# Kernel tuning notes

Hardware: AMD Instinct MI355X
Metric: run time of the kernel (lower is better)

The kernel has to match this reference:

```python
import jax, jax.numpy as jnp
import numpy as np
from jax import lax

B, C, H, W = 4, 32, 512, 512
DN = ('NCHW', 'OIHW', 'NCHW')

# cv2 correlation kernels (filter2D/Sobel/Scharr do correlation, not convolution)
SOBEL_X = np.array([[-1, 0, 1], [-2, 0, 2], [-1, 0, 1]], np.float32)
SOBEL_Y = SOBEL_X.T
SCHARR_X = np.array([[-3, 0, 3], [-10, 0, 10], [-3, 0, 3]], np.float32)
SCHARR_Y = SCHARR_X.T
LAPLACE3 = np.array([[2, 0, 2], [0, -8, 0], [2, 0, 2]], np.float32)  # cv2.Laplacian ksize=3
ROBERTS_X = np.array([[-1, 0], [0, 1]], np.float32)
ROBERTS_Y = np.array([[0, -1], [1, 0]], np.float32)
PREWITT_X = np.array([[1, 1, 1], [0, 0, 0], [-1, -1, -1]], np.float32)
PREWITT_Y = np.array([[-1, 0, 1], [-1, 0, 1], [-1, 0, 1]], np.float32)


def _corr(x, k, pad_hw):
    # per-channel 2D correlation with cv2 BORDER_REFLECT_101 padding
    b, c, h, w = x.shape
    xp = jnp.pad(x, ((0, 0), (0, 0), pad_hw[0], pad_hw[1]), mode='reflect')
    kj = jnp.asarray(k)[None, None]  # (1,1,kh,kw)
    y = lax.conv_general_dilated(xp.reshape(b * c, 1, xp.shape[2], xp.shape[3]),
                                 kj, (1, 1), 'VALID', dimension_numbers=DN)
    return y.reshape(b, c, h, w)


def _norm(x):
    # Norm(): per-sample zero-mean/unit-std over all of (C,H,W)
    m = jnp.mean(x, axis=(1, 2, 3), keepdims=True)
    s = jnp.std(x, axis=(1, 2, 3), keepdims=True)
    return (x - m) / s


def get_operator(x):
    p3 = ((1, 1), (1, 1))          # 3x3 kernel, anchor (1,1)
    p2 = ((1, 0), (1, 0))          # 2x2 kernel, cv2 default anchor (1,1)
    b1 = _norm(0.5 * _corr(x, SOBEL_X, p3) + 0.5 * _corr(x, SOBEL_Y, p3))
    b2 = _norm(0.5 * _corr(x, SCHARR_X, p3) + 0.5 * _corr(x, SCHARR_Y, p3))
    b3 = _norm(_corr(x, LAPLACE3, p3))
    b4 = _norm(0.5 * _corr(x, ROBERTS_X, p2) + 0.5 * _corr(x, ROBERTS_Y, p2))
    b5 = _norm(0.5 * _corr(x, PREWITT_X, p3) + 0.5 * _corr(x, PREWITT_Y, p3))
    return jnp.concatenate([b1, b2, b3, b4, b5], axis=1)


def conv3x3(x, w, b):
    y = lax.conv_general_dilated(x, w, (1, 1), [(1, 1), (1, 1)], dimension_numbers=DN)
    return y + b[None, :, None, None]


def maxpool2(x):
    b, c, h, w = x.shape
    return x.reshape(b, c, h // 2, 2, w // 2, 2).max(axis=(3, 5))


def deconv2x2(x, w, b):
    # ConvTranspose2d(k=2, s=2): each pixel expands to a 2x2 block; w is (Cin,Cout,2,2)
    bb, ci, h, wd = x.shape
    y = jnp.einsum('bihw,iopq->bohpwq', x, w).reshape(bb, w.shape[1], 2 * h, 2 * wd)
    return y + b[None, :, None, None]


def setup_inputs():
    key = jax.random.key(0)
    ks = jax.random.split(key, 24)
    def uni(k, shape, fan_in):
        bd = 1.0 / np.sqrt(fan_in)
        return jax.random.uniform(k, shape, jnp.float32, -bd, bd)
    d = {'x': jax.random.normal(ks[0], (B, C, H, W), jnp.float32)}
    d['conv1_w'] = uni(ks[1], (C, 5 * C, 3, 3), 5 * C * 9)
    d['conv1_b'] = uni(ks[2], (C,), 5 * C * 9)
    for i, name in enumerate(['conv2', 'conv3', 'conv4', 'conv5', 'conv6', 'conv7']):
        d[name + '_w'] = uni(ks[3 + 2 * i], (C, C, 3, 3), C * 9)
        d[name + '_b'] = uni(ks[4 + 2 * i], (C,), C * 9)
    for i, name in enumerate(['deconv1', 'deconv2', 'deconv3']):
        d[name + '_w'] = uni(ks[15 + 2 * i], (C, C, 2, 2), C * 4)
        d[name + '_b'] = uni(ks[16 + 2 * i], (C,), C * 4)
    return d


def reference(x, conv1_w, conv1_b, conv2_w, conv2_b, conv3_w, conv3_b, conv4_w, conv4_b,
              conv5_w, conv5_b, conv6_w, conv6_b, conv7_w, conv7_b,
              deconv1_w, deconv1_b, deconv2_w, deconv2_b, deconv3_w, deconv3_b):
    orig = x
    y = get_operator(x)                      # (B, 5C, H, W)
    y = conv3x3(y, conv1_w, conv1_b)
    y = maxpool2(y)
    y = conv3x3(y, conv2_w, conv2_b)
    y = maxpool2(y)
    y = conv3x3(y, conv3_w, conv3_b)
    y = maxpool2(y)
    y = conv3x3(y, conv4_w, conv4_b)
    y = deconv2x2(y, deconv1_w, deconv1_b)   # sizes divide evenly -> no interpolate
    y = conv3x3(y, conv5_w, conv5_b)
    y = deconv2x2(y, deconv2_w, deconv2_b)
    y = conv3x3(y, conv6_w, conv6_b)
    y = deconv2x2(y, deconv3_w, deconv3_b)
    y = conv3x3(y, conv7_w, conv7_b)
    return orig * y
```

## Files before the change

kernel.cpp:

```cpp
#include <hip/hip_runtime.h>
#include <hip/hip_bf16.h>
#include <cstddef>


typedef unsigned short u16;
typedef unsigned int uint;
typedef __attribute__((ext_vector_type(8))) short short8v;
typedef __attribute__((ext_vector_type(4))) float float4v;

constexpr int Bn = 4, Cn = 32, Hn = 512, Wn = 512;
constexpr int PLANE = Hn * Wn;

__device__ __forceinline__ u16 f2b(float f) {
  union { float f; uint i; } c; c.f = f;
  uint r = c.i + 0x7FFFu + ((c.i >> 16) & 1u);
  return (u16)(r >> 16);
}

static __device__ __forceinline__ int reflect_idx(int i, int n) {
  return i < 0 ? -i : (i >= n ? 2 * n - 2 - i : i);
}

#define BRANCH_VALS(n00, n01, n02, n10, n11, n12, n20, n21, n22, v1, v2, v3, v4, v5)        \
  do {                                                                                      \
    v1 = -(n00 + n01 + n10) + (n12 + n21 + n22);                                            \
    v2 = -3.f * n00 - 5.f * n01 - 5.f * n10 + 5.f * n12 + 5.f * n21 + 3.f * n22;            \
    v3 = 2.f * (n00 + n02 + n20 + n22) - 8.f * n11;                                         \
    v4 = 0.5f * (-n00 - n01 + n10 + n11);                                                   \
    v5 = 0.5f * n01 + n02 - 0.5f * n10 + 0.5f * n12 - n20 - 0.5f * n21;                     \
  } while (0)

__global__ void __launch_bounds__(128) k_opstats(const float* __restrict__ x,
                                                 float* __restrict__ partS,
                                                 float* __restrict__ partQ) {
  int bid = blockIdx.x;
  int b = bid >> 11;
  int local = bid & 2047;
  int c = local >> 6;
  int chunk = local & 63;
  int t = threadIdx.x;
  int w0 = t * 4;
  const float* xp = x + (size_t)(b * Cn + c) * PLANE;
  int h0 = chunk * 8;

  int ci[6];
#pragma unroll
  for (int j = 0; j < 6; j++) ci[j] = reflect_idx(w0 - 1 + j, Wn);

  float ap[6], ac[6], an[6];
  {
    const float* rp = xp + reflect_idx(h0 - 1, Hn) * Wn;
#pragma unroll
    for (int j = 0; j < 6; j++) ap[j] = rp[ci[j]];
  }
  {
    const float* rp = xp + h0 * Wn;
#pragma unroll
    for (int j = 0; j < 6; j++) ac[j] = rp[ci[j]];
  }

  float s[5] = {0, 0, 0, 0, 0}, q[5] = {0, 0, 0, 0, 0};
#pragma unroll
  for (int r = 0; r < 8; ++r) {
    int h = h0 + r;
    const float* rp = xp + reflect_idx(h + 1, Hn) * Wn;
#pragma unroll
    for (int j = 0; j < 6; j++) an[j] = rp[ci[j]];
#pragma unroll
    for (int k = 0; k < 4; ++k) {
      float v1, v2, v3, v4, v5;
      BRANCH_VALS(ap[k], ap[k + 1], ap[k + 2], ac[k], ac[k + 1], ac[k + 2],
                  an[k], an[k + 1], an[k + 2], v1, v2, v3, v4, v5);
      s[0] += v1; q[0] += v1 * v1;
      s[1] += v2; q[1] += v2 * v2;
      s[2] += v3; q[2] += v3 * v3;
      s[3] += v4; q[3] += v4 * v4;
      s[4] += v5; q[5 - 1] += v5 * v5;
    }
#pragma unroll
    for (int j = 0; j < 6; j++) { ap[j] = ac[j]; ac[j] = an[j]; }
  }

#pragma unroll
  for (int i = 0; i < 5; i++) {
    float ss = s[i], qq = q[i];
#pragma unroll
    for (int off = 32; off > 0; off >>= 1) {
      ss += __shfl_down(ss, off);
      qq += __shfl_down(qq, off);
    }
    if ((t & 63) == 0) {
      int wv = t >> 6;
      int g = b * 5 + i;
      int idx = (c * 64 + chunk) * 2 + wv;
      partS[(size_t)g * 4096 + idx] = ss;
      partQ[(size_t)g * 4096 + idx] = qq;
    }
  }
}

__global__ void __launch_bounds__(256) k_stats(const float* __restrict__ partS,
                                               const float* __restrict__ partQ,
                                               float* __restrict__ stats) {
  __shared__ float red[256];
  int g = blockIdx.x;
  int t = threadIdx.x;
  float ss = 0.f, qq = 0.f;
  const float* ps = partS + (size_t)g * 4096;
  const float* pq = partQ + (size_t)g * 4096;
  for (int i = t; i < 4096; i += 256) {
    ss += ps[i];
    qq += pq[i];
  }
  red[t] = ss;
  __syncthreads();
  for (int o = 128; o > 0; o >>= 1) {
    if (t < o) red[t] += red[t + o];
    __syncthreads();
  }
  float S = red[0];
  __syncthreads();
  red[t] = qq;
  __syncthreads();
  for (int o = 128; o > 0; o >>= 1) {
    if (t < o) red[t] += red[t + o];
    __syncthreads();
  }
  if (t == 0) {
    const float N = 8388608.0f;
    float mean = S / N;
    float var = red[0] / N - mean * mean;
    stats[g * 2] = mean;
    stats[g * 2 + 1] = 1.0f / sqrtf(var);
  }
}

__global__ void __launch_bounds__(256) k_opfused(const float* __restrict__ x, int b,
                                                 u16* __restrict__ opm) {
  __shared__ u16 lin[160 * 66];
  int t = threadIdx.x;
  int px = t & 63, cg = t >> 6;
  int h = blockIdx.y;
  int w = blockIdx.x * 64 + px;
  int hm = h == 0 ? 1 : h - 1, hp = h == 511 ? 510 : h + 1;
  int wm = w == 0 ? 1 : w - 1, wp = w == 511 ? 510 : w + 1;

#pragma unroll
  for (int it = 0; it < 8; ++it) {
    int c = it * 4 + cg;
    const float* xp = x + ((size_t)(b * 32 + c) * 512) * 512;
    const float* r0 = xp + (size_t)hm * 512;
    const float* r1 = xp + (size_t)h * 512;
    const float* r2 = xp + (size_t)hp * 512;
    float n00 = r0[wm], n01 = r0[w], n02 = r0[wp];
    float n10 = r1[wm], n11 = r1[w], n12 = r1[wp];
    float n20 = r2[wm], n21 = r2[w], n22 = r2[wp];
    float v1, v2, v3, v4, v5;
    BRANCH_VALS(n00, n01, n02, n10, n11, n12, n20, n21, n22, v1, v2, v3, v4, v5);
    lin[(c) * 66 + px] = f2b(v1);
    lin[(32 + c) * 66 + px] = f2b(v2);
    lin[(64 + c) * 66 + px] = f2b(v3);
    lin[(96 + c) * 66 + px] = f2b(v4);
    lin[(128 + c) * 66 + px] = f2b(v5);
  }
  __syncthreads();

  size_t obase = ((size_t)h * 512 + blockIdx.x * 64) * 160;
#pragma unroll
  for (int i = 0; i < 5; ++i) {
    int u = t + i * 256;
    int pxi = u / 20, chg = u % 20;
    u16 tmp[8];
#pragma unroll
    for (int j = 0; j < 8; ++j) tmp[j] = lin[(chg * 8 + j) * 66 + pxi];
    *(uint4*)&opm[obase + (size_t)pxi * 160 + chg * 8] = *(uint4*)tmp;
  }
}

__global__ void __launch_bounds__(256) k_prep_shared(
    const float* w2, const float* w3, const float* w4, const float* w5,
    const float* w6, const float* w7, const float* dw1, const float* dw2,
    const float* dw3, u16* A2, u16* A3, u16* A4, u16* A5, u16* A6, u16* A7,
    u16* Ad1, u16* Ad2, u16* Ad3) {
  int id = blockIdx.x * 256 + threadIdx.x;
  if (id < 55296) {
    int s = id / 9216, r = id % 9216;
    int tap = r / 1024, oc = (r >> 5) & 31, ic = r & 31;
    const float* w = s == 0 ? w2 : s == 1 ? w3 : s == 2 ? w4 : s == 3 ? w5 : s == 4 ? w6 : w7;
    u16* A = s == 0 ? A2 : s == 1 ? A3 : s == 2 ? A4 : s == 3 ? A5 : s == 4 ? A6 : A7;
    A[r] = f2b(w[(oc * 32 + ic) * 9 + tap]);
  } else if (id < 67584) {
    int r = id - 55296;
    int s = r / 4096, e = r % 4096;
    int par = e >> 10, oc = (e >> 5) & 31, ic = e & 31;
    const float* w = s == 0 ? dw1 : s == 1 ? dw2 : dw3;
    u16* A = s == 0 ? Ad1 : s == 1 ? Ad2 : Ad3;
    A[e] = f2b(w[(ic * 32 + oc) * 4 + par]);
  }
}

__global__ void __launch_bounds__(256) k_prep_b_all(const float* __restrict__ w1,
                                                    const float* __restrict__ b1,
                                                    const float* __restrict__ stats,
                                                    u16* __restrict__ A1all,
                                                    float* __restrict__ bias1all) {
  int e = blockIdx.x * 256 + threadIdx.x;
  if (e < 184320) {
    int b = e / 46080, r = e % 46080;
    int br = r / 9216, r2 = r % 9216;
    int tap = r2 / 1024, oc = (r2 >> 5) & 31, ic = r2 & 31;
    A1all[e] = f2b(w1[(oc * 160 + br * 32 + ic) * 9 + tap] * stats[(b * 5 + br) * 2 + 1]);
  } else if (e < 184448) {
    int t2 = e - 184320;
    int b = t2 >> 5, oc = t2 & 31;
    float s = 0.f;
    for (int ch = 0; ch < 160; ++ch) {
      int br = ch >> 5;
      float mi = stats[(b * 5 + br) * 2] * stats[(b * 5 + br) * 2 + 1];
      const float* wp = w1 + (size_t)(oc * 160 + ch) * 9;
      float ws = 0.f;
#pragma unroll
      for (int tap = 0; tap < 9; ++tap) ws += wp[tap];
      s += ws * mi;
    }
    bias1all[b * 32 + oc] = b1[oc] - s;
  }
}

template <int CIN, int MODE>
__global__ void __launch_bounds__(256) k_conv_mfma(const u16* __restrict__ in,
                                                   const u16* __restrict__ Aw,
                                                   const float* __restrict__ bias,
                                                   u16* __restrict__ outb,
                                                   float* __restrict__ outf,
                                                   const float* __restrict__ xorig,
                                                   int H, int W) {
  constexpr int ICC = CIN / 32;
  __shared__ __align__(16) char smem[(MODE == 1) ? 32768 : 20736];
  u16* bs = (u16*)smem;
  int t = threadIdx.x;
  int l = t & 63, wv = t >> 6;
  int ln = l & 15, q = l >> 4;
  int bz = blockIdx.z;
  int h0 = blockIdx.y * 16, w0 = blockIdx.x * 16;

  float4v acc[4][2];
#pragma unroll
  for (int i = 0; i < 4; ++i) {
    acc[i][0] = (float4v){0.f, 0.f, 0.f, 0.f};
    acc[i][1] = (float4v){0.f, 0.f, 0.f, 0.f};
  }

  for (int icc = 0; icc < ICC; ++icc) {
    for (int u = t; u < 1296; u += 256) {
      int px = u >> 2, sq = u & 3;
      int ry = px / 18, rx = px - ry * 18;
      int gh = h0 - 1 + ry, gw = w0 - 1 + rx;
      uint4 v = {0, 0, 0, 0};
      if (gh >= 0 && gh < H && gw >= 0 && gw < W)
        v = *(const uint4*)&in[(((size_t)bz * H + gh) * W + gw) * CIN + icc * 32 + sq * 8];
      *(uint4*)((char*)bs + px * 64 + ((sq ^ (px & 3)) << 4)) = v;
    }
    short8v af[9][2];
#pragma unroll
    for (int tp = 0; tp < 9; ++tp) {
      af[tp][0] = *(const short8v*)&Aw[((size_t)(icc * 9 + tp) * 32 + ln) * 32 + q * 8];
      af[tp][1] = *(const short8v*)&Aw[((size_t)(icc * 9 + tp) * 32 + 16 + ln) * 32 + q * 8];
    }
    __syncthreads();
#pragma unroll
    for (int r4 = 0; r4 < 4; ++r4) {
      int r = wv * 4 + r4;
#pragma unroll
      for (int dy = 0; dy < 3; ++dy) {
#pragma unroll
        for (int dx = 0; dx < 3; ++dx) {
          int px = (r + dy) * 18 + ln + dx;
          short8v bf = *(const short8v*)((const char*)bs + px * 64 + ((q ^ (px & 3)) << 4));
          acc[r4][0] = __builtin_amdgcn_mfma_f32_16x16x32_bf16(af[dy * 3 + dx][0], bf, acc[r4][0], 0, 0, 0);
          acc[r4][1] = __builtin_amdgcn_mfma_f32_16x16x32_bf16(af[dy * 3 + dx][1], bf, acc[r4][1], 0, 0, 0);
        }
      }
    }
    if (ICC > 1) __syncthreads();
  }

  if (MODE == 0) {
#pragma unroll
    for (int r4 = 0; r4 < 4; ++r4) {
      int h = h0 + wv * 4 + r4;
      int wpix = w0 + ln;
#pragma unroll
      for (int g = 0; g < 2; ++g) {
        float v0 = acc[r4][g][0] + bias[g * 16 + q * 4 + 0];
        float v1 = acc[r4][g][1] + bias[g * 16 + q * 4 + 1];
        float v2 = acc[r4][g][2] + bias[g * 16 + q * 4 + 2];
        float v3 = acc[r4][g][3] + bias[g * 16 + q * 4 + 3];
        uint2 pk;
        pk.x = (uint)f2b(v0) | ((uint)f2b(v1) << 16);
        pk.y = (uint)f2b(v2) | ((uint)f2b(v3) << 16);
        *(uint2*)&outb[(((size_t)bz * H + h) * W + wpix) * 32 + g * 16 + q * 4] = pk;
      }
    }
  } else if (MODE == 2) {
    int Hp = H >> 1, Wp = W >> 1;
#pragma unroll
    for (int rp = 0; rp < 2; ++rp) {
#pragma unroll
      for (int g = 0; g < 2; ++g) {
        float m0 = fmaxf(acc[2 * rp][g][0], acc[2 * rp + 1][g][0]);
        float m1 = fmaxf(acc[2 * rp][g][1], acc[2 * rp + 1][g][1]);
        float m2 = fmaxf(acc[2 * rp][g][2], acc[2 * rp + 1][g][2]);
        float m3 = fmaxf(acc[2 * rp][g][3], acc[2 * rp + 1][g][3]);
        m0 = fmaxf(m0, __shfl_xor(m0, 1));
        m1 = fmaxf(m1, __shfl_xor(m1, 1));
        m2 = fmaxf(m2, __shfl_xor(m2, 1));
        m3 = fmaxf(m3, __shfl_xor(m3, 1));
        if (!(l & 1)) {
          int ph = (h0 >> 1) + wv * 2 + rp;
          int pw = (w0 >> 1) + (ln >> 1);
          uint2 pk;
          pk.x = (uint)f2b(m0 + bias[g * 16 + q * 4 + 0]) |
                 ((uint)f2b(m1 + bias[g * 16 + q * 4 + 1]) << 16);
          pk.y = (uint)f2b(m2 + bias[g * 16 + q * 4 + 2]) |
                 ((uint)f2b(m3 + bias[g * 16 + q * 4 + 3]) << 16);
          *(uint2*)&outb[(((size_t)bz * Hp + ph) * Wp + pw) * 32 + g * 16 + q * 4] = pk;
        }
      }
    }
  } else {
    float* os = (float*)smem;
    __syncthreads();
#pragma unroll
    for (int r4 = 0; r4 < 4; ++r4) {
      int hl = wv * 4 + r4;
#pragma unroll
      for (int g = 0; g < 2; ++g) {
#pragma unroll
        for (int i = 0; i < 4; ++i) {
          int oc = g * 16 + q * 4 + i;
          os[(oc * 16 + hl) * 16 + ln] = acc[r4][g][i] + bias[oc];
        }
      }
    }
    __syncthreads();
#pragma unroll
    for (int j = 0; j < 8; ++j) {
      int u = t + j * 256;
      int wq = u & 3, hh = (u >> 2) & 15, oc = u >> 6;
      float4v v = *(const float4v*)&os[(oc * 16 + hh) * 16 + wq * 4];
      size_t gidx = (((size_t)bz * 32 + oc) * H + h0 + hh) * W + w0 + wq * 4;
      float4v xo = *(const float4v*)&xorig[gidx];
      v[0] *= xo[0]; v[1] *= xo[1]; v[2] *= xo[2]; v[3] *= xo[3];
      *(float4v*)&outf[gidx] = v;
    }
  }
}

__global__ void __launch_bounds__(256) k_deconv_mfma(const u16* __restrict__ in,
                                                     const u16* __restrict__ Aw,
                                                     const float* __restrict__ bias,
                                                     u16* __restrict__ out,
                                                     int Hi, int Wi) {
  int t = threadIdx.x;
  int l = t & 63, wv = t >> 6, ln = l & 15, q = l >> 4;
  int z = blockIdx.z, b = z >> 2, par = z & 3, p = par >> 1, qpar = par & 1;
  int h0 = blockIdx.y * 16, w0 = blockIdx.x * 16;
  int Ho = Hi * 2, Wo = Wi * 2;
  short8v af0 = *(const short8v*)&Aw[((size_t)par * 32 + ln) * 32 + q * 8];
  short8v af1 = *(const short8v*)&Aw[((size_t)par * 32 + 16 + ln) * 32 + q * 8];
#pragma unroll
  for (int r4 = 0; r4 < 4; ++r4) {
    int h = h0 + wv * 4 + r4;
    short8v bf = *(const short8v*)&in[(((size_t)b * Hi + h) * Wi + w0 + ln) * 32 + q * 8];
    float4v a0 = (float4v){0.f, 0.f, 0.f, 0.f};
    float4v a1 = (float4v){0.f, 0.f, 0.f, 0.f};
    a0 = __builtin_amdgcn_mfma_f32_16x16x32_bf16(af0, bf, a0, 0, 0, 0);
    a1 = __builtin_amdgcn_mfma_f32_16x16x32_bf16(af1, bf, a1, 0, 0, 0);
    int oh = 2 * h + p, ow = 2 * (w0 + ln) + qpar;
    size_t ob = (((size_t)b * Ho + oh) * Wo + ow) * 32;
    uint2 pk;
    pk.x = (uint)f2b(a0[0] + bias[q * 4 + 0]) | ((uint)f2b(a0[1] + bias[q * 4 + 1]) << 16);
    pk.y = (uint)f2b(a0[2] + bias[q * 4 + 2]) | ((uint)f2b(a0[3] + bias[q * 4 + 3]) << 16);
    *(uint2*)&out[ob + q * 4] = pk;
    pk.x = (uint)f2b(a1[0] + bias[16 + q * 4 + 0]) | ((uint)f2b(a1[1] + bias[16 + q * 4 + 1]) << 16);
    pk.y = (uint)f2b(a1[2] + bias[16 + q * 4 + 2]) | ((uint)f2b(a1[3] + bias[16 + q * 4 + 3]) << 16);
    *(uint2*)&out[ob + 16 + q * 4] = pk;
  }
}

extern "C" void kernel_launch(void* const* d_in, const int* in_sizes, int n_in,
                              void* d_out, int out_size, void* d_ws, size_t ws_size,
                              hipStream_t stream) {
  const float* x   = (const float*)d_in[0];
  const float* w1  = (const float*)d_in[1];
  const float* b1  = (const float*)d_in[2];
  const float* w2  = (const float*)d_in[3];
  const float* b2  = (const float*)d_in[4];
  const float* w3  = (const float*)d_in[5];
  const float* b3  = (const float*)d_in[6];
  const float* w4  = (const float*)d_in[7];
  const float* b4  = (const float*)d_in[8];
  const float* w5  = (const float*)d_in[9];
  const float* b5  = (const float*)d_in[10];
  const float* w6  = (const float*)d_in[11];
  const float* b6  = (const float*)d_in[12];
  const float* w7  = (const float*)d_in[13];
  const float* b7  = (const float*)d_in[14];
  const float* dw1 = (const float*)d_in[15];
  const float* db1 = (const float*)d_in[16];
  const float* dw2 = (const float*)d_in[17];
  const float* db2 = (const float*)d_in[18];
  const float* dw3 = (const float*)d_in[19];
  const float* db3 = (const float*)d_in[20];
  float* out = (float*)d_out;
  char* wsb = (char*)d_ws;

  u16* opm   = (u16*)(wsb + 0);
  u16* p1    = (u16*)(wsb + 83886080ull);
  u16* p2    = (u16*)(wsb + 100663296ull);
  u16* p3    = (u16*)(wsb + 104857600ull);
  u16* t4    = (u16*)(wsb + 105906176ull);
  u16* dc1   = (u16*)(wsb + 106954752ull);
  u16* t5    = (u16*)(wsb + 111149056ull);
  u16* dc2   = (u16*)(wsb + 115343360ull);
  u16* t6    = (u16*)(wsb + 132120576ull);
  u16* dc3   = (u16*)(wsb + 148897792ull);
  u16* A1all = (u16*)(wsb + 216006656ull);
  u16* A2    = (u16*)(wsb + 216375296ull);
  u16* A3    = (u16*)(wsb + 216393728ull);
  u16* A4    = (u16*)(wsb + 216412160ull);
  u16* A5    = (u16*)(wsb + 216430592ull);
  u16* A6    = (u16*)(wsb + 216449024ull);
  u16* A7    = (u16*)(wsb + 216467456ull);
  u16* Ad1   = (u16*)(wsb + 216485888ull);
  u16* Ad2   = (u16*)(wsb + 216494080ull);
  u16* Ad3   = (u16*)(wsb + 216502272ull);
  float* bias1all = (float*)(wsb + 216510464ull);
  float* partS    = (float*)(wsb + 216510976ull);
  float* partQ    = (float*)(wsb + 216838656ull);
  float* stats    = (float*)(wsb + 217166336ull);

  k_prep_shared<<<264, 256, 0, stream>>>(w2, w3, w4, w5, w6, w7, dw1, dw2, dw3,
                                         A2, A3, A4, A5, A6, A7, Ad1, Ad2, Ad3);
  k_opstats<<<8192, 128, 0, stream>>>(x, partS, partQ);
  k_stats<<<20, 256, 0, stream>>>(partS, partQ, stats);
  k_prep_b_all<<<721, 256, 0, stream>>>(w1, b1, stats, A1all, bias1all);

  for (int b = 0; b < 4; ++b) {
    k_opfused<<<dim3(8, 512), 256, 0, stream>>>(x, b, opm);
    k_conv_mfma<160, 2><<<dim3(32, 32, 1), 256, 0, stream>>>(
        opm, A1all + (size_t)b * 46080, bias1all + b * 32,
        p1 + (size_t)b * 256 * 256 * 32, nullptr, nullptr, 512, 512);
  }

  k_conv_mfma<32, 2><<<dim3(16, 16, 4), 256, 0, stream>>>(p1, A2, b2, p2, nullptr, nullptr, 256, 256);
  k_conv_mfma<32, 2><<<dim3(8, 8, 4), 256, 0, stream>>>(p2, A3, b3, p3, nullptr, nullptr, 128, 128);
  k_conv_mfma<32, 0><<<dim3(4, 4, 4), 256, 0, stream>>>(p3, A4, b4, t4, nullptr, nullptr, 64, 64);
  k_deconv_mfma<<<dim3(4, 4, 16), 256, 0, stream>>>(t4, Ad1, db1, dc1, 64, 64);
  k_conv_mfma<32, 0><<<dim3(8, 8, 4), 256, 0, stream>>>(dc1, A5, b5, t5, nullptr, nullptr, 128, 128);
  k_deconv_mfma<<<dim3(8, 8, 16), 256, 0, stream>>>(t5, Ad2, db2, dc2, 128, 128);
  k_conv_mfma<32, 0><<<dim3(16, 16, 4), 256, 0, stream>>>(dc2, A6, b6, t6, nullptr, nullptr, 256, 256);
  k_deconv_mfma<<<dim3(16, 16, 16), 256, 0, stream>>>(t6, Ad3, db3, dc3, 256, 256);
  k_conv_mfma<32, 1><<<dim3(32, 32, 4), 256, 0, stream>>>(dc3, A7, b7, nullptr, out, x, 512, 512);
}
```

Baseline: 791.0 us.

## Fold edge-operator branches into conv1 as a single 5x5 conv on input

The five fixed edge filters are composed algebraically with conv1's 3x3 weights into one 5x5 kernel (32→32 channels) per batch, so conv1 reads x directly instead of materialising the 160-channel bf16 operator map. Normalization is folded into the weights and bias. Border pixels, where the composition does not hold, are recomputed exactly by a separate scalar kernel that overwrites them. The final conv's epilogue now stages output in two halves to reduce shared memory. This removes a large intermediate write and read, but relies on the separate border correction and changes rounding, since weights are composed before the bf16 cast.

```diff
diff --git a/kernel.cpp b/kernel.cpp
--- a/kernel.cpp
+++ b/kernel.cpp
@@ -11,6 +11,9 @@
 constexpr int Bn = 4, Cn = 32, Hn = 512, Wn = 512;
 constexpr int PLANE = Hn * Wn;
 
+__device__ __forceinline__ float b2f(u16 u) {
+  union { uint i; float f; } c; c.i = ((uint)u) << 16; return c.f;
+}
 __device__ __forceinline__ u16 f2b(float f) {
   union { float f; uint i; } c; c.f = f;
   uint r = c.i + 0x7FFFu + ((c.i >> 16) & 1u);
@@ -29,6 +32,13 @@
     v4 = 0.5f * (-n00 - n01 + n10 + n11);                                                   \
     v5 = 0.5f * n01 + n02 - 0.5f * n10 + 0.5f * n12 - n20 - 0.5f * n21;                     \
   } while (0)
+
+__device__ const float Sdev[5][9] = {
+    {-1.f, -1.f, 0.f, -1.f, 0.f, 1.f, 0.f, 1.f, 1.f},
+    {-3.f, -5.f, 0.f, -5.f, 0.f, 5.f, 0.f, 5.f, 3.f},
+    {2.f, 0.f, 2.f, 0.f, -8.f, 0.f, 2.f, 0.f, 2.f},
+    {-0.5f, -0.5f, 0.f, 0.5f, 0.5f, 0.f, 0.f, 0.f, 0.f},
+    {0.f, 0.5f, 1.f, -0.5f, 0.f, 0.5f, -1.f, -0.5f, 0.f}};
 
 __global__ void __launch_bounds__(128) k_opstats(const float* __restrict__ x,
                                                  float* __restrict__ partS,
@@ -75,7 +85,7 @@
       s[1] += v2; q[1] += v2 * v2;
       s[2] += v3; q[2] += v3 * v3;
       s[3] += v4; q[3] += v4 * v4;
-      s[4] += v5; q[5 - 1] += v5 * v5;
+      s[4] += v5; q[4] += v5 * v5;
     }
 #pragma unroll
     for (int j = 0; j < 6; j++) { ap[j] = ac[j]; ac[j] = an[j]; }
@@ -132,48 +142,6 @@
     float var = red[0] / N - mean * mean;
     stats[g * 2] = mean;
     stats[g * 2 + 1] = 1.0f / sqrtf(var);
-  }
-}
-
-__global__ void __launch_bounds__(256) k_opfused(const float* __restrict__ x, int b,
-                                                 u16* __restrict__ opm) {
-  __shared__ u16 lin[160 * 66];
-  int t = threadIdx.x;
-  int px = t & 63, cg = t >> 6;
-  int h = blockIdx.y;
-  int w = blockIdx.x * 64 + px;
-  int hm = h == 0 ? 1 : h - 1, hp = h == 511 ? 510 : h + 1;
-  int wm = w == 0 ? 1 : w - 1, wp = w == 511 ? 510 : w + 1;
-
-#pragma unroll
-  for (int it = 0; it < 8; ++it) {
-    int c = it * 4 + cg;
-    const float* xp = x + ((size_t)(b * 32 + c) * 512) * 512;
-    const float* r0 = xp + (size_t)hm * 512;
-    const float* r1 = xp + (size_t)h * 512;
-    const float* r2 = xp + (size_t)hp * 512;
-    float n00 = r0[wm], n01 = r0[w], n02 = r0[wp];
-    float n10 = r1[wm], n11 = r1[w], n12 = r1[wp];
-    float n20 = r2[wm], n21 = r2[w], n22 = r2[wp];
-    float v1, v2, v3, v4, v5;
-    BRANCH_VALS(n00, n01, n02, n10, n11, n12, n20, n21, n22, v1, v2, v3, v4, v5);
-    lin[(c) * 66 + px] = f2b(v1);
-    lin[(32 + c) * 66 + px] = f2b(v2);
-    lin[(64 + c) * 66 + px] = f2b(v3);
-    lin[(96 + c) * 66 + px] = f2b(v4);
-    lin[(128 + c) * 66 + px] = f2b(v5);
-  }
-  __syncthreads();
-
-  size_t obase = ((size_t)h * 512 + blockIdx.x * 64) * 160;
-#pragma unroll
-  for (int i = 0; i < 5; ++i) {
-    int u = t + i * 256;
-    int pxi = u / 20, chg = u % 20;
-    u16 tmp[8];
-#pragma unroll
-    for (int j = 0; j < 8; ++j) tmp[j] = lin[(chg * 8 + j) * 66 + pxi];
-    *(uint4*)&opm[obase + (size_t)pxi * 160 + chg * 8] = *(uint4*)tmp;
   }
 }
 
@@ -199,19 +167,38 @@
   }
 }
 
-__global__ void __launch_bounds__(256) k_prep_b_all(const float* __restrict__ w1,
+__global__ void __launch_bounds__(256) k_prep_conv1(const float* __restrict__ w1,
                                                     const float* __restrict__ b1,
                                                     const float* __restrict__ stats,
-                                                    u16* __restrict__ A1all,
+                                                    u16* __restrict__ A5c,
                                                     float* __restrict__ bias1all) {
   int e = blockIdx.x * 256 + threadIdx.x;
-  if (e < 184320) {
-    int b = e / 46080, r = e % 46080;
-    int br = r / 9216, r2 = r % 9216;
-    int tap = r2 / 1024, oc = (r2 >> 5) & 31, ic = r2 & 31;
-    A1all[e] = f2b(w1[(oc * 160 + br * 32 + ic) * 9 + tap] * stats[(b * 5 + br) * 2 + 1]);
-  } else if (e < 184448) {
-    int t2 = e - 184320;
+  if (e < 102400) {
+    int b = e / 25600, r = e % 25600;
+    int tap = r >> 10, oc = (r >> 5) & 31, ic = r & 31;
+    int u = tap / 5, v = tap % 5;
+    float acc = 0.f;
+#pragma unroll
+    for (int br = 0; br < 5; ++br) {
+      float is = stats[(b * 5 + br) * 2 + 1];
+      const float* wp = w1 + ((size_t)oc * 160 + br * 32 + ic) * 9;
+      float sub = 0.f;
+#pragma unroll
+      for (int a = 0; a < 3; ++a) {
+        int s = u - a;
+        if (s < 0 || s > 2) continue;
+#pragma unroll
+        for (int bb = 0; bb < 3; ++bb) {
+          int tt = v - bb;
+          if (tt < 0 || tt > 2) continue;
+          sub += wp[a * 3 + bb] * Sdev[br][s * 3 + tt];
+        }
+      }
+      acc += is * sub;
+    }
+    A5c[e] = f2b(acc);
+  } else if (e < 102528) {
+    int t2 = e - 102400;
     int b = t2 >> 5, oc = t2 & 31;
     float s = 0.f;
     for (int ch = 0; ch < 160; ++ch) {
@@ -225,6 +212,176 @@
     }
     bias1all[b * 32 + oc] = b1[oc] - s;
   }
+}
+
+__global__ void __launch_bounds__(256) k_conv5x5(const float* __restrict__ x,
+                                                 const u16* __restrict__ A5c,
+                                                 const float* __restrict__ biasAll,
+                                                 u16* __restrict__ outb) {
+  __shared__ __align__(16) u16 bs[400 * 32];
+  int t = threadIdx.x;
+  int l = t & 63, wv = t >> 6, ln = l & 15, q = l >> 4;
+  int b = blockIdx.z;
+  int h0 = blockIdx.y * 16, w0 = blockIdx.x * 16;
+
+  {
+    int cp = t & 15;
+    int px0 = t >> 4;
+    int py = 0, pxx = px0;
+    const float* xp0 = x + ((size_t)b * 32 + 2 * cp) * PLANE;
+    const float* xp1 = xp0 + PLANE;
+#pragma unroll
+    for (int i = 0; i < 25; ++i) {
+      int gh = reflect_idx(h0 - 2 + py, Hn);
+      int gw = reflect_idx(w0 - 2 + pxx, Wn);
+      float v0 = xp0[gh * Wn + gw];
+      float v1 = xp1[gh * Wn + gw];
+      int px = py * 20 + pxx;
+      uint pk = (uint)f2b(v0) | ((uint)f2b(v1) << 16);
+      *(uint*)((char*)bs + px * 64 + ((((cp >> 2) ^ (px & 3)) << 4)) + (cp & 3) * 4) = pk;
+      pxx += 16;
+      if (pxx >= 20) { pxx -= 20; py += 1; }
+    }
+  }
+  __syncthreads();
+
+  float4v acc[4][2];
+#pragma unroll
+  for (int i = 0; i < 4; ++i) {
+    acc[i][0] = (float4v){0.f, 0.f, 0.f, 0.f};
+    acc[i][1] = (float4v){0.f, 0.f, 0.f, 0.f};
+  }
+
+  const u16* Ab = A5c + (size_t)b * 25600;
+#pragma unroll
+  for (int ty = 0; ty < 5; ++ty) {
+#pragma unroll
+    for (int tx = 0; tx < 5; ++tx) {
+      int tap = ty * 5 + tx;
+      short8v af0 = *(const short8v*)&Ab[((size_t)tap * 32 + ln) * 32 + q * 8];
+      short8v af1 = *(const short8v*)&Ab[((size_t)tap * 32 + 16 + ln) * 32 + q * 8];
+#pragma unroll
+      for (int r4 = 0; r4 < 4; ++r4) {
+        int px = (wv * 4 + r4 + ty) * 20 + ln + tx;
+        short8v bf = *(const short8v*)((const char*)bs + px * 64 + ((q ^ (px & 3)) << 4));
+        acc[r4][0] = __builtin_amdgcn_mfma_f32_16x16x32_bf16(af0, bf, acc[r4][0], 0, 0, 0);
+        acc[r4][1] = __builtin_amdgcn_mfma_f32_16x16x32_bf16(af1, bf, acc[r4][1], 0, 0, 0);
+      }
+    }
+  }
+
+  const float* bias = biasAll + b * 32;
+#pragma unroll
+  for (int rp = 0; rp < 2; ++rp) {
+#pragma unroll
+    for (int g = 0; g < 2; ++g) {
+      float m0 = fmaxf(acc[2 * rp][g][0], acc[2 * rp + 1][g][0]);
+      float m1 = fmaxf(acc[2 * rp][g][1], acc[2 * rp + 1][g][1]);
+      float m2 = fmaxf(acc[2 * rp][g][2], acc[2 * rp + 1][g][2]);
+      float m3 = fmaxf(acc[2 * rp][g][3], acc[2 * rp + 1][g][3]);
+      m0 = fmaxf(m0, __shfl_xor(m0, 1));
+      m1 = fmaxf(m1, __shfl_xor(m1, 1));
+      m2 = fmaxf(m2, __shfl_xor(m2, 1));
+      m3 = fmaxf(m3, __shfl_xor(m3, 1));
+      if (!(l & 1)) {
+        int ph = (h0 >> 1) + wv * 2 + rp;
+        int pw = (w0 >> 1) + (ln >> 1);
+        uint2 pk;
+        pk.x = (uint)f2b(m0 + bias[g * 16 + q * 4 + 0]) |
+               ((uint)f2b(m1 + bias[g * 16 + q * 4 + 1]) << 16);
+        pk.y = (uint)f2b(m2 + bias[g * 16 + q * 4 + 2]) |
+               ((uint)f2b(m3 + bias[g * 16 + q * 4 + 3]) << 16);
+        *(uint2*)&outb[(((size_t)b * 256 + ph) * 256 + pw) * 32 + g * 16 + q * 4] = pk;
+      }
+    }
+  }
+}
+
+__global__ void __launch_bounds__(256) k_border(const float* __restrict__ x,
+                                                const float* __restrict__ w1,
+                                                const float* __restrict__ b1,
+                                                const float* __restrict__ stats,
+                                                u16* __restrict__ p1) {
+  int t = threadIdx.x;
+  int lane = t & 63, quad = t >> 6;
+  int b = blockIdx.y;
+  int p = blockIdx.x * 64 + lane;
+  if (p >= 4080) return;
+  int cell = p >> 2, k = p & 3;
+  int ph, pw;
+  if (cell < 256) { ph = 0; pw = cell; }
+  else if (cell < 512) { ph = 255; pw = cell - 256; }
+  else if (cell < 766) { ph = 1 + (cell - 512); pw = 0; }
+  else { ph = 1 + (cell - 766); pw = 255; }
+  int h = 2 * ph + (k >> 1), w = 2 * pw + (k & 1);
+
+  float mean[5], istd[5];
+#pragma unroll
+  for (int br = 0; br < 5; ++br) {
+    mean[br] = stats[(b * 5 + br) * 2];
+    istd[br] = stats[(b * 5 + br) * 2 + 1];
+  }
+
+  float acc[8];
+#pragma unroll
+  for (int i = 0; i < 8; ++i) acc[i] = 0.f;
+
+  for (int c = 0; c < 32; ++c) {
+    const float* xp = x + (size_t)(b * 32 + c) * PLANE;
+    float xw[5][5];
+#pragma unroll
+    for (int dy = 0; dy < 5; ++dy) {
+      int gh = reflect_idx(h - 2 + dy, Hn);
+#pragma unroll
+      for (int dx = 0; dx < 5; ++dx) {
+        int gw = reflect_idx(w - 2 + dx, Wn);
+        xw[dy][dx] = xp[gh * Wn + gw];
+      }
+    }
+    float Bnv[5][9];
+#pragma unroll
+    for (int ty = 0; ty < 3; ++ty) {
+#pragma unroll
+      for (int tx = 0; tx < 3; ++tx) {
+        int hh = h + ty - 1, ww = w + tx - 1;
+        bool valid = (hh >= 0 && hh < Hn && ww >= 0 && ww < Wn);
+        float v1, v2, v3, v4, v5;
+        BRANCH_VALS(xw[ty][tx], xw[ty][tx + 1], xw[ty][tx + 2],
+                    xw[ty + 1][tx], xw[ty + 1][tx + 1], xw[ty + 1][tx + 2],
+                    xw[ty + 2][tx], xw[ty + 2][tx + 1], xw[ty + 2][tx + 2],
+                    v1, v2, v3, v4, v5);
+        int tap = ty * 3 + tx;
+        Bnv[0][tap] = valid ? (v1 - mean[0]) * istd[0] : 0.f;
+        Bnv[1][tap] = valid ? (v2 - mean[1]) * istd[1] : 0.f;
+        Bnv[2][tap] = valid ? (v3 - mean[2]) * istd[2] : 0.f;
+        Bnv[3][tap] = valid ? (v4 - mean[3]) * istd[3] : 0.f;
+        Bnv[4][tap] = valid ? (v5 - mean[4]) * istd[4] : 0.f;
+      }
+    }
+#pragma unroll
+    for (int br = 0; br < 5; ++br) {
+#pragma unroll
+      for (int oc8 = 0; oc8 < 8; ++oc8) {
+        int oc = quad * 8 + oc8;
+        const float* wp = w1 + ((size_t)oc * 160 + br * 32 + c) * 9;
+        float a0 = acc[oc8];
+#pragma unroll
+        for (int tap = 0; tap < 9; ++tap) a0 = fmaf(wp[tap], Bnv[br][tap], a0);
+        acc[oc8] = a0;
+      }
+    }
+  }
+
+  u16 r[8];
+#pragma unroll
+  for (int oc8 = 0; oc8 < 8; ++oc8) {
+    float m = acc[oc8] + b1[quad * 8 + oc8];
+    m = fmaxf(m, __shfl_xor(m, 1));
+    m = fmaxf(m, __shfl_xor(m, 2));
+    r[oc8] = f2b(m);
+  }
+  if (k == 0)
+    *(uint4*)&p1[(((size_t)b * 256 + ph) * 256 + pw) * 32 + quad * 8] = *(uint4*)r;
 }
 
 template <int CIN, int MODE>
@@ -236,7 +393,7 @@
                                                    const float* __restrict__ xorig,
                                                    int H, int W) {
   constexpr int ICC = CIN / 32;
-  __shared__ __align__(16) char smem[(MODE == 1) ? 32768 : 20736];
+  __shared__ __align__(16) char smem[20736];
   u16* bs = (u16*)smem;
   int t = threadIdx.x;
   int l = t & 63, wv = t >> 6;
@@ -330,29 +487,29 @@
     }
   } else {
     float* os = (float*)smem;
-    __syncthreads();
-#pragma unroll
-    for (int r4 = 0; r4 < 4; ++r4) {
-      int hl = wv * 4 + r4;
-#pragma unroll
-      for (int g = 0; g < 2; ++g) {
+#pragma unroll
+    for (int g = 0; g < 2; ++g) {
+      __syncthreads();
+#pragma unroll
+      for (int r4 = 0; r4 < 4; ++r4) {
+        int hl = wv * 4 + r4;
 #pragma unroll
         for (int i = 0; i < 4; ++i) {
-          int oc = g * 16 + q * 4 + i;
-          os[(oc * 16 + hl) * 16 + ln] = acc[r4][g][i] + bias[oc];
+          int ocl = q * 4 + i;
+          os[(ocl * 16 + hl) * 20 + ln] = acc[r4][g][i] + bias[g * 16 + ocl];
         }
       }
-    }
-    __syncthreads();
-#pragma unroll
-    for (int j = 0; j < 8; ++j) {
-      int u = t + j * 256;
-      int wq = u & 3, hh = (u >> 2) & 15, oc = u >> 6;
-      float4v v = *(const float4v*)&os[(oc * 16 + hh) * 16 + wq * 4];
-      size_t gidx = (((size_t)bz * 32 + oc) * H + h0 + hh) * W + w0 + wq * 4;
-      float4v xo = *(const float4v*)&xorig[gidx];
-      v[0] *= xo[0]; v[1] *= xo[1]; v[2] *= xo[2]; v[3] *= xo[3];
-      *(float4v*)&outf[gidx] = v;
+      __syncthreads();
+#pragma unroll
+      for (int j = 0; j < 4; ++j) {
+        int u = t + j * 256;
+        int wq = u & 3, hh = (u >> 2) & 15, ocl = u >> 6;
+        float4v v = *(const float4v*)&os[(ocl * 16 + hh) * 20 + wq * 4];
+        size_t gidx = (((size_t)bz * 32 + g * 16 + ocl) * H + h0 + hh) * W + w0 + wq * 4;
+        float4v xo = *(const float4v*)&xorig[gidx];
+        v[0] *= xo[0]; v[1] *= xo[1]; v[2] *= xo[2]; v[3] *= xo[3];
+        *(float4v*)&outf[gidx] = v;
+      }
     }
   }
 }
@@ -416,43 +573,38 @@
   float* out = (float*)d_out;
   char* wsb = (char*)d_ws;
 
-  u16* opm   = (u16*)(wsb + 0);
-  u16* p1    = (u16*)(wsb + 83886080ull);
-  u16* p2    = (u16*)(wsb + 100663296ull);
-  u16* p3    = (u16*)(wsb + 104857600ull);
-  u16* t4    = (u16*)(wsb + 105906176ull);
-  u16* dc1   = (u16*)(wsb + 106954752ull);
-  u16* t5    = (u16*)(wsb + 111149056ull);
-  u16* dc2   = (u16*)(wsb + 115343360ull);
-  u16* t6    = (u16*)(wsb + 132120576ull);
-  u16* dc3   = (u16*)(wsb + 148897792ull);
-  u16* A1all = (u16*)(wsb + 216006656ull);
-  u16* A2    = (u16*)(wsb + 216375296ull);
-  u16* A3    = (u16*)(wsb + 216393728ull);
-  u16* A4    = (u16*)(wsb + 216412160ull);
-  u16* A5    = (u16*)(wsb + 216430592ull);
-  u16* A6    = (u16*)(wsb + 216449024ull);
-  u16* A7    = (u16*)(wsb + 216467456ull);
-  u16* Ad1   = (u16*)(wsb + 216485888ull);
-  u16* Ad2   = (u16*)(wsb + 216494080ull);
-  u16* Ad3   = (u16*)(wsb + 216502272ull);
-  float* bias1all = (float*)(wsb + 216510464ull);
-  float* partS    = (float*)(wsb + 216510976ull);
-  float* partQ    = (float*)(wsb + 216838656ull);
-  float* stats    = (float*)(wsb + 217166336ull);
+  u16* p1  = (u16*)(wsb + 0);
+  u16* p2  = (u16*)(wsb + 16777216ull);
+  u16* p3  = (u16*)(wsb + 20971520ull);
+  u16* t4  = (u16*)(wsb + 22020096ull);
+  u16* dc1 = (u16*)(wsb + 23068672ull);
+  u16* t5  = (u16*)(wsb + 27262976ull);
+  u16* dc2 = (u16*)(wsb + 31457280ull);
+  u16* t6  = (u16*)(wsb + 48234496ull);
+  u16* dc3 = (u16*)(wsb + 65011712ull);
+  u16* A5c = (u16*)(wsb + 132120576ull);
+  u16* A2  = (u16*)(wsb + 132325376ull);
+  u16* A3  = (u16*)(wsb + 132343808ull);
+  u16* A4  = (u16*)(wsb + 132362240ull);
+  u16* A5  = (u16*)(wsb + 132380672ull);
+  u16* A6  = (u16*)(wsb + 132399104ull);
+  u16* A7  = (u16*)(wsb + 132417536ull);
+  u16* Ad1 = (u16*)(wsb + 132435968ull);
+  u16* Ad2 = (u16*)(wsb + 132444160ull);
+  u16* Ad3 = (u16*)(wsb + 132452352ull);
+  float* bias1all = (float*)(wsb + 132460544ull);
+  float* partS    = (float*)(wsb + 132461056ull);
+  float* partQ    = (float*)(wsb + 132788736ull);
+  float* stats    = (float*)(wsb + 133116416ull);
 
   k_prep_shared<<<264, 256, 0, stream>>>(w2, w3, w4, w5, w6, w7, dw1, dw2, dw3,
                                          A2, A3, A4, A5, A6, A7, Ad1, Ad2, Ad3);
   k_opstats<<<8192, 128, 0, stream>>>(x, partS, partQ);
   k_stats<<<20, 256, 0, stream>>>(partS, partQ, stats);
-  k_prep_b_all<<<721, 256, 0, stream>>>(w1, b1, stats, A1all, bias1all);
-
-  for (int b = 0; b < 4; ++b) {
-    k_opfused<<<dim3(8, 512), 256, 0, stream>>>(x, b, opm);
-    k_conv_mfma<160, 2><<<dim3(32, 32, 1), 256, 0, stream>>>(
-        opm, A1all + (size_t)b * 46080, bias1all + b * 32,
-        p1 + (size_t)b * 256 * 256 * 32, nullptr, nullptr, 512, 512);
-  }
+  k_prep_conv1<<<401, 256, 0, stream>>>(w1, b1, stats, A5c, bias1all);
+
+  k_conv5x5<<<dim3(32, 32, 4), 256, 0, stream>>>(x, A5c, bias1all, p1);
+  k_border<<<dim3(64, 4), 256, 0, stream>>>(x, w1, b1, stats, p1);
 
   k_conv_mfma<32, 2><<<dim3(16, 16, 4), 256, 0, stream>>>(p1, A2, b2, p2, nullptr, nullptr, 256, 256);
   k_conv_mfma<32, 2><<<dim3(8, 8, 4), 256, 0, stream>>>(p2, A3, b3, p3, nullptr, nullptr, 128, 128);
```

After: 847.4 us. 7.1% more time.
